# Kernel tuning notes

Hardware: AMD Instinct MI355X
Metric: run time of the kernel (lower is better)

Reference implementation:

```python
import jax, jax.numpy as jnp
import numpy as np

DIM = 33
EPS = 1e-5

def _conv(x, w, b, stride, pad):
    y = jax.lax.conv_general_dilated(x, w, (stride, stride), [(pad, pad), (pad, pad)],
                                     dimension_numbers=('NCHW', 'OIHW', 'NCHW'))
    return y + b[None, :, None, None]

def _lrelu(x):
    return jnp.where(x >= 0, x, 0.2 * x)

def _inorm(x, g, b):
    m = x.mean(axis=(2, 3), keepdims=True)
    v = x.var(axis=(2, 3), keepdims=True)
    return (x - m) * jax.lax.rsqrt(v + EPS) * g[None, :, None, None] + b[None, :, None, None]

def _classifier(img, w1, b1, g1, be1, w2, b2, g2, be2, w3, b3, g3, be3,
                w4, b4, g4, be4, w5, b5, w6, b6):
    x = jax.image.resize(img, (img.shape[0], 3, 256, 256), method='bilinear')
    x = _inorm(_lrelu(_conv(x, w1, b1, 2, 1)), g1, be1)   # [B,16,128,128]
    x = _inorm(_lrelu(_conv(x, w2, b2, 2, 1)), g2, be2)   # [B,32,64,64]
    x = _inorm(_lrelu(_conv(x, w3, b3, 2, 1)), g3, be3)   # [B,64,32,32]
    x = _inorm(_lrelu(_conv(x, w4, b4, 2, 1)), g4, be4)   # [B,128,16,16]
    x = _lrelu(_conv(x, w5, b5, 2, 1))                     # [B,128,8,8]
    x = _conv(x, w6, b6, 1, 0)                             # [B,3,1,1]
    return x.reshape(-1)                                   # squeeze (B=1) -> [3]

def _trilinear(lut, img):
    # lut: [3, dim, dim, dim] indexed [c, b_idx, g_idx, r_idx]; img: [B,3,H,W] in [0,1]
    scale = DIM - 1
    x = img * scale
    idx = jnp.clip(jnp.floor(x), 0, DIM - 2).astype(jnp.int32)
    f = x - idx                                            # fractional weights (differentiable in img)
    ir, ig, ib = idx[:, 0], idx[:, 1], idx[:, 2]           # [B,H,W]
    fr, fg, fb = f[:, 0], f[:, 1], f[:, 2]
    out = jnp.zeros((3,) + ir.shape, dtype=img.dtype)
    for db in (0, 1):
        wb = fb if db else 1.0 - fb
        for dg in (0, 1):
            wg = fg if dg else 1.0 - fg
            for dr in (0, 1):
                wr = fr if dr else 1.0 - fr
                corner = lut[:, ib + db, ig + dg, ir + dr]  # [3,B,H,W] gather
                out = out + (wb * wg * wr)[None] * corner
    return jnp.transpose(out, (1, 0, 2, 3))                # [B,3,H,W]

def _forward(image_input, lut0, lut1, lut2, w1, b1, g1, be1, w2, b2, g2, be2,
             w3, b3, g3, be3, w4, b4, g4, be4, w5, b5, w6, b6):
    pred = _classifier(image_input, w1, b1, g1, be1, w2, b2, g2, be2, w3, b3, g3, be3,
                       w4, b4, g4, be4, w5, b5, w6, b6)
    final_lut = pred[0] * lut0 + pred[1] * lut1 + pred[2] * lut2
    return _trilinear(final_lut, image_input)

def setup_inputs() -> dict:
    key = jax.random.key(0)
    ks = jax.random.split(key, 16)
    B, H, W = 1, 2160, 3840
    d = {}
    d['image_input'] = jax.random.uniform(ks[0], (B, 3, H, W), dtype=jnp.float32)
    d['lut0'] = jax.random.normal(ks[1], (3, DIM, DIM, DIM), dtype=jnp.float32)
    d['lut1'] = jax.random.normal(ks[2], (3, DIM, DIM, DIM), dtype=jnp.float32)
    d['lut2'] = jax.random.normal(ks[3], (3, DIM, DIM, DIM), dtype=jnp.float32)
    s = 0.05
    d['w1'] = jax.random.normal(ks[4], (16, 3, 3, 3), dtype=jnp.float32) * s
    d['b1'] = jnp.zeros((16,), jnp.float32); d['g1'] = jnp.ones((16,), jnp.float32); d['be1'] = jnp.zeros((16,), jnp.float32)
    d['w2'] = jax.random.normal(ks[5], (32, 16, 3, 3), dtype=jnp.float32) * s
    d['b2'] = jnp.zeros((32,), jnp.float32); d['g2'] = jnp.ones((32,), jnp.float32); d['be2'] = jnp.zeros((32,), jnp.float32)
    d['w3'] = jax.random.normal(ks[6], (64, 32, 3, 3), dtype=jnp.float32) * s
    d['b3'] = jnp.zeros((64,), jnp.float32); d['g3'] = jnp.ones((64,), jnp.float32); d['be3'] = jnp.zeros((64,), jnp.float32)
    d['w4'] = jax.random.normal(ks[7], (128, 64, 3, 3), dtype=jnp.float32) * s
    d['b4'] = jnp.zeros((128,), jnp.float32); d['g4'] = jnp.ones((128,), jnp.float32); d['be4'] = jnp.zeros((128,), jnp.float32)
    d['w5'] = jax.random.normal(ks[8], (128, 128, 3, 3), dtype=jnp.float32) * s
    d['b5'] = jnp.zeros((128,), jnp.float32)
    d['w6'] = jax.random.normal(ks[9], (3, 128, 8, 8), dtype=jnp.float32) * s
    d['b6'] = jnp.zeros((3,), jnp.float32)
    return d

def reference(image_input, lut0, lut1, lut2, w1, b1, g1, be1, w2, b2, g2, be2,
              w3, b3, g3, be3, w4, b4, g4, be4, w5, b5, w6, b6):
    return _forward(image_input, lut0, lut1, lut2, w1, b1, g1, be1, w2, b2, g2, be2,
                    w3, b3, g3, be3, w4, b4, g4, be4, w5, b5, w6, b6)
```

## Files before the change

### kernel.cpp

```cpp
#include <hip/hip_runtime.h>

#define NPX (2160*3840)
#define EPS 1e-5f

typedef float __attribute__((ext_vector_type(4))) fx4;

__global__ void resize_w_kernel(const float* __restrict__ img, float* __restrict__ tmp) {
  __shared__ __align__(16) float row[3840];
  const int bh = blockIdx.x;
  const float* src = img + (size_t)bh * 3840;
  const int tid = threadIdx.x;
  const float4* s4 = (const float4*)src;
  float4* r4 = (float4*)row;
  for (int i = tid; i < 960; i += 256) r4[i] = s4[i];
  __syncthreads();
  const int i = tid;
  const int center = 15*i + 7;
  int lo = center - 14; if (lo < 0) lo = 0;
  int hi = center + 14; if (hi > 3839) hi = 3839;
  float acc = 0.f, wsum = 0.f;
  for (int j = lo; j <= hi; ++j) {
    int d = center - j; d = d < 0 ? -d : d;
    float w = (float)(15 - d);
    acc += w * row[j];
    wsum += w;
  }
  tmp[bh*256 + i] = acc / wsum;
}

__global__ void resize_h_kernel(const float* __restrict__ tmp, float* __restrict__ dst) {
  const int c = blockIdx.x >> 8;
  const int oh = blockIdx.x & 255;
  const int ow = threadIdx.x;
  const float sf = ((float)oh + 0.5f) * 8.4375f - 0.5f;
  int lo = (int)ceilf(sf - 8.4375f); if (lo < 0) lo = 0;
  int hi = (int)floorf(sf + 8.4375f); if (hi > 2159) hi = 2159;
  float acc = 0.f, wsum = 0.f;
  for (int j = lo; j <= hi; ++j) {
    float w = 1.f - fabsf(sf - (float)j) * (16.f/135.f);
    if (w > 0.f) {
      acc += w * tmp[(c*2160 + j)*256 + ow];
      wsum += w;
    }
  }
  dst[blockIdx.x*256 + ow] = acc / wsum;
}

template<int CIN,int CICHUNK,int HIN,int WIN,int HOUT,int WOUT,int NPIN,int MODE>
__global__ __launch_bounds__(256) void conv_fused(
    const float* __restrict__ in, const float* __restrict__ wt, const float* __restrict__ bias,
    const float* __restrict__ pin, const float* __restrict__ gin, const float* __restrict__ bin,
    float* __restrict__ out, float* __restrict__ pout,
    const float* __restrict__ gself, const float* __restrict__ bself) {
  constexpr int NTW = WOUT/16;
  constexpr int NT  = (HOUT/16)*NTW;
  constexpr int NCHUNK = CIN/CICHUNK;
  constexpr int SLOTS = CICHUNK*33*9;
  constexpr float PHW_INV = 1.f/(float)(HIN*WIN);

  __shared__ float sx[CICHUNK*33*36];
  __shared__ float wl[CIN*9];
  __shared__ float sA[CIN], sB[CIN];
  __shared__ float2 red2[256];

  const int co = blockIdx.x / NT;
  const int t  = blockIdx.x % NT;
  const int oh0 = (t / NTW)*16, ow0 = (t % NTW)*16;
  const int tid = threadIdx.x;

  for (int i = tid; i < CIN*9; i += 256) wl[i] = wt[co*CIN*9 + i];
  if (NPIN > 0) {
    if (tid < CIN) {
      const float2* p2 = (const float2*)pin;
      float s = 0.f, q = 0.f;
      #pragma unroll 4
      for (int k = 0; k < NPIN; ++k) { float2 p = p2[tid*NPIN + k]; s += p.x; q += p.y; }
      const float m = s * PHW_INV;
      float var = q * PHW_INV - m*m; var = fmaxf(var, 0.f);
      const float A = gin[tid] * rsqrtf(var + EPS);
      sA[tid] = A; sB[tid] = bin[tid] - m*A;
    }
  }
  __syncthreads();

  const int ohl = tid >> 4, owl = tid & 15;
  float acc = bias[co];

  for (int cc = 0; cc < NCHUNK; ++cc) {
    if (cc) __syncthreads();
    const int cb = cc*CICHUNK;
    for (int i = tid; i < SLOTS; i += 256) {
      const int ci_l = i / 297;
      const int rem  = i - ci_l*297;
      const int r = rem / 9, q = rem - r*9;
      const int grow = 2*oh0 - 1 + r;
      const int ga   = 2*ow0 - 4 + 4*q;
      float4 v = make_float4(0.f,0.f,0.f,0.f);
      if (grow >= 0 && grow < HIN && ga >= 0) {
        v = *(const float4*)(in + ((size_t)(cb+ci_l)*HIN + grow)*WIN + ga);
        if (NPIN > 0) {
          const float A = sA[cb+ci_l], B = sB[cb+ci_l];
          v.x = fmaf(A, v.x, B); v.y = fmaf(A, v.y, B);
          v.z = fmaf(A, v.z, B); v.w = fmaf(A, v.w, B);
        }
      }
      *(float4*)&sx[(ci_l*33 + r)*36 + q*4] = v;
    }
    __syncthreads();
    #pragma unroll 4
    for (int ci_l = 0; ci_l < CICHUNK; ++ci_l) {
      const float* sp = sx + ci_l*1188;
      const float* wp = wl + (cb+ci_l)*9;
      #pragma unroll
      for (int kh = 0; kh < 3; ++kh) {
        const float* rp = sp + (2*ohl + kh)*36 + 3 + 2*owl;
        acc = fmaf(rp[0], wp[kh*3+0], acc);
        acc = fmaf(rp[1], wp[kh*3+1], acc);
        acc = fmaf(rp[2], wp[kh*3+2], acc);
      }
    }
  }

  acc = acc >= 0.f ? acc : 0.2f*acc;
  out[(size_t)co*HOUT*WOUT + (oh0+ohl)*WOUT + ow0 + owl] = acc;

  red2[tid] = make_float2(acc, acc*acc);
  __syncthreads();
  for (int s = 128; s > 0; s >>= 1) {
    if (tid < s) { red2[tid].x += red2[tid+s].x; red2[tid].y += red2[tid+s].y; }
    __syncthreads();
  }
  if (tid == 0) {
    if (MODE == 1) {
      ((float2*)pout)[co*NT + t] = red2[0];
    } else {
      const float m = red2[0].x / (float)(HOUT*WOUT);
      float var = red2[0].y / (float)(HOUT*WOUT) - m*m; var = fmaxf(var, 0.f);
      const float A = gself[co] * rsqrtf(var + EPS);
      pout[co*2]   = A;
      pout[co*2+1] = bself[co] - m*A;
    }
  }
}

__global__ __launch_bounds__(256) void conv5_fused(const float* __restrict__ in,
    const float* __restrict__ wt, const float* __restrict__ bias,
    const float* __restrict__ ab4, const float* __restrict__ w6,
    float* __restrict__ part) {
  __shared__ float sx[32*17*20];
  __shared__ float wl[128*9];
  __shared__ float sA[128], sB[128];
  __shared__ float red[256];
  const int co = blockIdx.x;
  const int tid = threadIdx.x;
  for (int i = tid; i < 1152; i += 256) wl[i] = wt[co*1152 + i];
  if (tid < 128) { sA[tid] = ab4[tid*2]; sB[tid] = ab4[tid*2+1]; }
  __syncthreads();

  const int px = tid & 63, q = tid >> 6;
  const int ohl = px >> 3, owl = px & 7;
  float acc = 0.f;
  for (int cc = 0; cc < 4; ++cc) {
    if (cc) __syncthreads();
    const int cb = cc*32;
    for (int i = tid; i < 32*17*5; i += 256) {
      const int ci_l = i / 85;
      const int rem  = i - ci_l*85;
      const int r = rem / 5, qq = rem - r*5;
      const int grow = r - 1;
      const int ga   = 4*qq - 4;
      float4 v = make_float4(0.f,0.f,0.f,0.f);
      if (grow >= 0 && grow < 16 && ga >= 0) {
        v = *(const float4*)(in + ((size_t)(cb+ci_l)*16 + grow)*16 + ga);
        const float A = sA[cb+ci_l], B = sB[cb+ci_l];
        v.x = fmaf(A, v.x, B); v.y = fmaf(A, v.y, B);
        v.z = fmaf(A, v.z, B); v.w = fmaf(A, v.w, B);
      }
      *(float4*)&sx[(ci_l*17 + r)*20 + qq*4] = v;
    }
    __syncthreads();
    #pragma unroll 2
    for (int k = 0; k < 8; ++k) {
      const int ci_l = q*8 + k;
      const float* sp = sx + ci_l*340;
      const float* wp = wl + (cb+ci_l)*9;
      #pragma unroll
      for (int kh = 0; kh < 3; ++kh) {
        const float* rp = sp + (2*ohl + kh)*20 + 3 + 2*owl;
        acc = fmaf(rp[0], wp[kh*3+0], acc);
        acc = fmaf(rp[1], wp[kh*3+1], acc);
        acc = fmaf(rp[2], wp[kh*3+2], acc);
      }
    }
  }
  red[tid] = acc;
  __syncthreads();
  if (tid < 64) {
    float a = red[tid] + red[tid+64] + red[tid+128] + red[tid+192] + bias[co];
    a = a >= 0.f ? a : 0.2f*a;
    #pragma unroll
    for (int j = 0; j < 3; ++j) {
      float v = a * w6[(j*128 + co)*64 + tid];
      #pragma unroll
      for (int off = 32; off > 0; off >>= 1) v += __shfl_down(v, off);
      if (tid == 0) part[co*3 + j] = v;
    }
  }
}

__global__ __launch_bounds__(256) void blend_pack_kernel(const float* __restrict__ l0,
    const float* __restrict__ l1, const float* __restrict__ l2,
    const float* __restrict__ part, const float* __restrict__ b6,
    unsigned* __restrict__ flp) {
  __shared__ float sp[3];
  const int tid = threadIdx.x;
  if (tid < 3) {
    float s = b6[tid];
    #pragma unroll 16
    for (int k = 0; k < 128; ++k) s += part[k*3 + tid];
    sp[tid] = s;
  }
  __syncthreads();
  const int i = blockIdx.x*256 + tid;
  if (i >= 3*35936) return;
  const int c = i / 35936, j = i - c*35936;
  const int src = c*35937 + j;
  const float v0 = sp[0]*l0[src]   + sp[1]*l1[src]   + sp[2]*l2[src];
  const float v1 = sp[0]*l0[src+1] + sp[1]*l1[src+1] + sp[2]*l2[src+1];
  unsigned u0 = __float_as_uint(v0); u0 = (u0 + 0x7fffu + ((u0>>16)&1u)) >> 16;
  unsigned u1 = __float_as_uint(v1); u1 = (u1 + 0x7fffu + ((u1>>16)&1u)) >> 16;
  flp[c*35936 + j] = u0 | (u1 << 16);
}

__global__ __launch_bounds__(1024) void trilinear_kernel(const float* __restrict__ img,
    const unsigned* __restrict__ flp, float* __restrict__ out) {
  __shared__ unsigned slut[35936];
  const int tid = threadIdx.x;
  const int p0 = blockIdx.x * 32400;
  for (int c = 0; c < 3; ++c) {
    if (c) __syncthreads();
    for (int i = tid; i < 35936; i += 1024) slut[i] = flp[c*35936 + i];
    __syncthreads();
    for (int g = tid; g < 8100; g += 1024) {
      const int p = p0 + 4*g;
      const float4 rr = *(const float4*)(img + p);
      const float4 gg = *(const float4*)(img + NPX + p);
      const float4 bb = *(const float4*)(img + 2*NPX + p);
      const float rv[4] = {rr.x, rr.y, rr.z, rr.w};
      const float gv[4] = {gg.x, gg.y, gg.z, gg.w};
      const float bv[4] = {bb.x, bb.y, bb.z, bb.w};
      float ov[4];
      #pragma unroll
      for (int k = 0; k < 4; ++k) {
        const float xr = rv[k]*32.f, xg = gv[k]*32.f, xb = bv[k]*32.f;
        int ir = (int)xr; ir = ir > 31 ? 31 : ir;
        int ig = (int)xg; ig = ig > 31 ? 31 : ig;
        int ib = (int)xb; ib = ib > 31 ? 31 : ib;
        const float fr = xr - (float)ir;
        const float fg = xg - (float)ig;
        const float fb = xb - (float)ib;
        const int base = (ib*33 + ig)*33 + ir;
        const unsigned p00 = slut[base],      p01 = slut[base+33];
        const unsigned p10 = slut[base+1089], p11 = slut[base+1122];
        const float v000 = __uint_as_float(p00 << 16), v001 = __uint_as_float(p00 & 0xffff0000u);
        const float v010 = __uint_as_float(p01 << 16), v011 = __uint_as_float(p01 & 0xffff0000u);
        const float v100 = __uint_as_float(p10 << 16), v101 = __uint_as_float(p10 & 0xffff0000u);
        const float v110 = __uint_as_float(p11 << 16), v111 = __uint_as_float(p11 & 0xffff0000u);
        const float a0 = fmaf(fr, v001 - v000, v000);
        const float a1 = fmaf(fr, v011 - v010, v010);
        const float a2 = fmaf(fr, v101 - v100, v100);
        const float a3 = fmaf(fr, v111 - v110, v110);
        const float lo = fmaf(fg, a1 - a0, a0);
        const float hi = fmaf(fg, a3 - a2, a2);
        ov[k] = fmaf(fb, hi - lo, lo);
      }
      fx4 res = {ov[0], ov[1], ov[2], ov[3]};
      __builtin_nontemporal_store(res, (fx4*)(out + (size_t)c*NPX + p));
    }
  }
}

extern "C" void kernel_launch(void* const* d_in, const int* in_sizes, int n_in,
                              void* d_out, int out_size, void* d_ws, size_t ws_size,
                              hipStream_t stream) {
  const float* img  = (const float*)d_in[0];
  const float* lut0 = (const float*)d_in[1];
  const float* lut1 = (const float*)d_in[2];
  const float* lut2 = (const float*)d_in[3];
  const float* w1 = (const float*)d_in[4];  const float* b1  = (const float*)d_in[5];
  const float* g1 = (const float*)d_in[6];  const float* be1 = (const float*)d_in[7];
  const float* w2 = (const float*)d_in[8];  const float* b2  = (const float*)d_in[9];
  const float* g2 = (const float*)d_in[10]; const float* be2 = (const float*)d_in[11];
  const float* w3 = (const float*)d_in[12]; const float* b3  = (const float*)d_in[13];
  const float* g3 = (const float*)d_in[14]; const float* be3 = (const float*)d_in[15];
  const float* w4 = (const float*)d_in[16]; const float* b4  = (const float*)d_in[17];
  const float* g4 = (const float*)d_in[18]; const float* be4 = (const float*)d_in[19];
  const float* w5 = (const float*)d_in[20]; const float* b5  = (const float*)d_in[21];
  const float* w6 = (const float*)d_in[22]; const float* b6  = (const float*)d_in[23];

  float* ws = (float*)d_ws;
  float* tmp   = ws;
  float* r256  = ws + 1658880;
  float* c1    = ws;
  float* c2    = ws + 262144;
  float* c3    = ws + 393216;
  float* c4    = ws + 458752;
  float* part1 = ws + 491520;
  float* part2 = ws + 493568;
  float* part3 = ws + 494592;
  float* ab4   = ws + 495104;
  float* part6 = ws + 495360;
  unsigned* flp = (unsigned*)(ws + 495872);

  resize_w_kernel<<<3*2160, 256, 0, stream>>>(img, tmp);
  resize_h_kernel<<<3*256, 256, 0, stream>>>(tmp, r256);

  conv_fused< 3, 3,256,256,128,128, 0,1><<<16*64, 256, 0, stream>>>(
      r256, w1, b1, nullptr, nullptr, nullptr, c1, part1, nullptr, nullptr);
  conv_fused<16,16,128,128, 64, 64,64,1><<<32*16, 256, 0, stream>>>(
      c1, w2, b2, part1, g1, be1, c2, part2, nullptr, nullptr);
  conv_fused<32,32, 64, 64, 32, 32,16,1><<<64*4, 256, 0, stream>>>(
      c2, w3, b3, part2, g2, be2, c3, part3, nullptr, nullptr);
  conv_fused<64,32, 32, 32, 16, 16, 4,2><<<128, 256, 0, stream>>>(
      c3, w4, b4, part3, g3, be3, c4, ab4, g4, be4);
  conv5_fused<<<128, 256, 0, stream>>>(c4, w5, b5, ab4, w6, part6);

  blend_pack_kernel<<<422, 256, 0, stream>>>(lut0, lut1, lut2, part6, b6, flp);
  trilinear_kernel<<<256, 1024, 0, stream>>>(img, flp, (float*)d_out);
}
```

Baseline: 198.8 us.

## Unroll resize taps, use wavefront shuffle reductions, and vectorize LUT loads

The width resize now pads the shared row with zeros so each thread runs a fixed, fully unrolled 29-tap FMA loop, and it divides by a constant reciprocal in place of a bounds-clamped loop with a running weight sum. The height resize drops its weight>0 branch. The conv kernel's 256-entry shared tree reduction is replaced by wavefront shuffles plus a 4-way shared combine, and blend_pack sums its 128 partials in parallel with shuffles. The trilinear kernel loads the LUT into shared memory as uint4. These mainly trim per-block sync and loop overhead, and they rely on the fixed image sizes and on the height weights never going non-positive.

```diff
diff --git a/kernel.cpp b/kernel.cpp
--- a/kernel.cpp
+++ b/kernel.cpp
@@ -5,30 +5,31 @@
 
 typedef float __attribute__((ext_vector_type(4))) fx4;
 
-__global__ void resize_w_kernel(const float* __restrict__ img, float* __restrict__ tmp) {
-  __shared__ __align__(16) float row[3840];
+__global__ __launch_bounds__(256) void resize_w_kernel(const float* __restrict__ img,
+                                                       float* __restrict__ tmp) {
+  __shared__ __align__(16) float row[3872];
   const int bh = blockIdx.x;
   const float* src = img + (size_t)bh * 3840;
   const int tid = threadIdx.x;
+  if (tid < 16) { row[tid] = 0.f; row[3856 + tid] = 0.f; }
   const float4* s4 = (const float4*)src;
-  float4* r4 = (float4*)row;
+  float4* r4 = (float4*)(row + 16);
   for (int i = tid; i < 960; i += 256) r4[i] = s4[i];
   __syncthreads();
   const int i = tid;
-  const int center = 15*i + 7;
-  int lo = center - 14; if (lo < 0) lo = 0;
-  int hi = center + 14; if (hi > 3839) hi = 3839;
-  float acc = 0.f, wsum = 0.f;
-  for (int j = lo; j <= hi; ++j) {
-    int d = center - j; d = d < 0 ? -d : d;
-    float w = (float)(15 - d);
-    acc += w * row[j];
-    wsum += w;
-  }
-  tmp[bh*256 + i] = acc / wsum;
-}
-
-__global__ void resize_h_kernel(const float* __restrict__ tmp, float* __restrict__ dst) {
+  const float* rp = row + 15*i + 9;
+  float acc = 0.f;
+  #pragma unroll
+  for (int k = 0; k < 29; ++k) {
+    const float w = (float)(15 - (k < 14 ? 14 - k : k - 14));
+    acc = fmaf(w, rp[k], acc);
+  }
+  const float rcpw = (i == 0 || i == 255) ? (1.f/197.f) : (1.f/225.f);
+  tmp[bh*256 + i] = acc * rcpw;
+}
+
+__global__ __launch_bounds__(256) void resize_h_kernel(const float* __restrict__ tmp,
+                                                       float* __restrict__ dst) {
   const int c = blockIdx.x >> 8;
   const int oh = blockIdx.x & 255;
   const int ow = threadIdx.x;
@@ -37,11 +38,9 @@
   int hi = (int)floorf(sf + 8.4375f); if (hi > 2159) hi = 2159;
   float acc = 0.f, wsum = 0.f;
   for (int j = lo; j <= hi; ++j) {
-    float w = 1.f - fabsf(sf - (float)j) * (16.f/135.f);
-    if (w > 0.f) {
-      acc += w * tmp[(c*2160 + j)*256 + ow];
-      wsum += w;
-    }
+    const float w = 1.f - fabsf(sf - (float)j) * (16.f/135.f);
+    acc = fmaf(w, tmp[(c*2160 + j)*256 + ow], acc);
+    wsum += w;
   }
   dst[blockIdx.x*256 + ow] = acc / wsum;
 }
@@ -61,7 +60,7 @@
   __shared__ float sx[CICHUNK*33*36];
   __shared__ float wl[CIN*9];
   __shared__ float sA[CIN], sB[CIN];
-  __shared__ float2 red2[256];
+  __shared__ float2 wred[4];
 
   const int co = blockIdx.x / NT;
   const int t  = blockIdx.x % NT;
@@ -124,18 +123,22 @@
   acc = acc >= 0.f ? acc : 0.2f*acc;
   out[(size_t)co*HOUT*WOUT + (oh0+ohl)*WOUT + ow0 + owl] = acc;
 
-  red2[tid] = make_float2(acc, acc*acc);
-  __syncthreads();
-  for (int s = 128; s > 0; s >>= 1) {
-    if (tid < s) { red2[tid].x += red2[tid+s].x; red2[tid].y += red2[tid+s].y; }
-    __syncthreads();
-  }
+  float s = acc, q = acc*acc;
+  #pragma unroll
+  for (int off = 32; off > 0; off >>= 1) {
+    s += __shfl_down(s, off);
+    q += __shfl_down(q, off);
+  }
+  if ((tid & 63) == 0) wred[tid >> 6] = make_float2(s, q);
+  __syncthreads();
   if (tid == 0) {
+    const float S = wred[0].x + wred[1].x + wred[2].x + wred[3].x;
+    const float Q = wred[0].y + wred[1].y + wred[2].y + wred[3].y;
     if (MODE == 1) {
-      ((float2*)pout)[co*NT + t] = red2[0];
+      ((float2*)pout)[co*NT + t] = make_float2(S, Q);
     } else {
-      const float m = red2[0].x / (float)(HOUT*WOUT);
-      float var = red2[0].y / (float)(HOUT*WOUT) - m*m; var = fmaxf(var, 0.f);
+      const float m = S / (float)(HOUT*WOUT);
+      float var = Q / (float)(HOUT*WOUT) - m*m; var = fmaxf(var, 0.f);
       const float A = gself[co] * rsqrtf(var + EPS);
       pout[co*2]   = A;
       pout[co*2+1] = bself[co] - m*A;
@@ -212,14 +215,22 @@
     const float* __restrict__ l1, const float* __restrict__ l2,
     const float* __restrict__ part, const float* __restrict__ b6,
     unsigned* __restrict__ flp) {
+  __shared__ float sred[2][3];
   __shared__ float sp[3];
   const int tid = threadIdx.x;
-  if (tid < 3) {
-    float s = b6[tid];
-    #pragma unroll 16
-    for (int k = 0; k < 128; ++k) s += part[k*3 + tid];
-    sp[tid] = s;
-  }
+  float a0 = 0.f, a1 = 0.f, a2 = 0.f;
+  if (tid < 128) { a0 = part[tid*3]; a1 = part[tid*3+1]; a2 = part[tid*3+2]; }
+  #pragma unroll
+  for (int off = 32; off > 0; off >>= 1) {
+    a0 += __shfl_down(a0, off);
+    a1 += __shfl_down(a1, off);
+    a2 += __shfl_down(a2, off);
+  }
+  if (tid < 128 && (tid & 63) == 0) {
+    sred[tid >> 6][0] = a0; sred[tid >> 6][1] = a1; sred[tid >> 6][2] = a2;
+  }
+  __syncthreads();
+  if (tid < 3) sp[tid] = sred[0][tid] + sred[1][tid] + b6[tid];
   __syncthreads();
   const int i = blockIdx.x*256 + tid;
   if (i >= 3*35936) return;
@@ -239,7 +250,11 @@
   const int p0 = blockIdx.x * 32400;
   for (int c = 0; c < 3; ++c) {
     if (c) __syncthreads();
-    for (int i = tid; i < 35936; i += 1024) slut[i] = flp[c*35936 + i];
+    {
+      uint4* d4 = (uint4*)slut;
+      const uint4* s4 = (const uint4*)(flp + c*35936);
+      for (int i = tid; i < 8984; i += 1024) d4[i] = s4[i];
+    }
     __syncthreads();
     for (int g = tid; g < 8100; g += 1024) {
       const int p = p0 + 4*g;
```

After: 194.4 us. 2.2% less time.
